# Kernel optimization log

Measured on AMD Instinct MI355X. Metric: run time of the kernel, lower is better.

## Reference

```python
import jax, jax.numpy as jnp
import numpy as np

# ---- config (matches init_kwargs) ----
B, S, V = 8, 900, 11
H, NH, HD = 512, 8, 64          # hidden, heads, head_dim = H // NH
L = 2                            # num_layers
EXPANSION = 4.0
INNER = 1536                     # find_multiple(round(4.0 * 512 * 2/3), 256)
STEPS = 2                        # mcmc_num_steps
EPS = 1e-5                       # rms_norm_eps
THETA = 10000.0                  # rope_theta
ESCALE = float(np.sqrt(H))       # embed_scale = sqrt(hidden_size)
SCALE = 1.0 / float(np.sqrt(HD))


def rms_norm(x):
    return x * jax.lax.rsqrt(jnp.mean(x * x, axis=-1, keepdims=True) + EPS)


def rope_tables():
    inv_freq = 1.0 / (THETA ** (jnp.arange(0, HD, 2, dtype=jnp.float32) / HD))
    t = jnp.arange(S, dtype=jnp.float32)
    freqs = jnp.outer(t, inv_freq)                # (S, HD/2)
    emb = jnp.concatenate([freqs, freqs], axis=-1)  # (S, HD)
    return jnp.cos(emb), jnp.sin(emb)


def rotate_half(x):
    x1, x2 = jnp.split(x, 2, axis=-1)
    return jnp.concatenate([-x2, x1], axis=-1)


def apply_rope(q, k, cos, sin):
    cos = cos[None, :, None, :]  # (1,S,1,HD) broadcast over batch & heads
    sin = sin[None, :, None, :]
    return q * cos + rotate_half(q) * sin, k * cos + rotate_half(k) * sin


def block(h, qkv_w, o_w, gu_w, d_w, cos, sin):
    b, s, _ = h.shape
    qkv = (h @ qkv_w).reshape(b, s, 3 * NH, HD)
    q, k, v = qkv[:, :, :NH], qkv[:, :, NH:2 * NH], qkv[:, :, 2 * NH:]
    q, k = apply_rope(q, k, cos, sin)
    scores = jnp.einsum('bqhd,bkhd->bhqk', q, k) * SCALE
    attn = jax.nn.softmax(scores, axis=-1)
    out = jnp.einsum('bhqk,bkhd->bqhd', attn, v).reshape(b, s, NH * HD)
    h = rms_norm(h + out @ o_w)                   # post-norm residual
    gu = h @ gu_w
    gate, up = gu[..., :INNER], gu[..., INNER:]
    h = rms_norm(h + (jax.nn.silu(gate) * up) @ d_w)
    return h


def energy(logits, embed_w, energy_w, qkv_w, o_w, gu_w, d_w, input_emb, cos, sin):
    probs = jax.nn.softmax(logits, axis=-1)       # soft token distribution
    h = input_emb + ESCALE * (probs @ embed_w)    # soft embedding
    for i in range(L):
        h = block(h, qkv_w[i], o_w[i], gu_w[i], d_w[i], cos, sin)
    return jnp.sum(h @ energy_w)                  # scalar energy


def setup_inputs() -> dict:
    key = jax.random.key(0)
    ks = jax.random.split(key, 8)
    inputs = jax.random.randint(ks[0], (B, S), 0, V, dtype=jnp.int64)
    puzzle_identifiers = jax.random.randint(ks[1], (B,), 0, 1, dtype=jnp.int64)
    init_std = 1.0 / ESCALE
    embed_w = jax.random.normal(ks[2], (V, H), jnp.float32) * init_std
    energy_w = jax.random.normal(ks[3], (H, 1), jnp.float32) * 0.02
    qkv_w = jax.random.normal(ks[4], (L, H, 3 * NH * HD), jnp.float32) * 0.02
    o_w = jax.random.normal(ks[5], (L, NH * HD, H), jnp.float32) * 0.02
    gu_w = jax.random.normal(ks[6], (L, H, 2 * INNER), jnp.float32) * 0.02
    d_w = jax.random.normal(ks[7], (L, INNER, H), jnp.float32) * 0.02
    alpha = jnp.asarray(100.0, jnp.float32)       # mcmc_step_size
    return {"inputs": inputs, "puzzle_identifiers": puzzle_identifiers,
            "embed_w": embed_w, "energy_w": energy_w, "qkv_w": qkv_w,
            "o_w": o_w, "gu_w": gu_w, "d_w": d_w, "alpha": alpha}


def reference(inputs, puzzle_identifiers, embed_w, energy_w, qkv_w, o_w, gu_w, d_w, alpha):
    cos, sin = rope_tables()
    input_emb = ESCALE * embed_w[inputs]          # (B,S,H)
    a = jnp.maximum(alpha, 1e-4)                  # torch.clamp(alpha, min=1e-4)
    logits = jnp.zeros((inputs.shape[0], S, V), jnp.float32)
    egrad = jax.grad(energy)
    for _ in range(STEPS):                        # MCMC energy-descent loop
        g = egrad(logits, embed_w, energy_w, qkv_w, o_w, gu_w, d_w, input_emb, cos, sin)
        logits = logits - a * g
    return logits
```

## Files before the change

### kernel.cpp

```cpp
#include <hip/hip_runtime.h>
#include <math.h>

#define B_ 8
#define S_ 900
#define V_ 11
#define H_ 512
#define NH_ 8
#define HD_ 64
#define INNER_ 1536
#define STEPS_ 2
#define NTOK (B_*S_)
#define EPS_ 1e-5f
#define THETA_ 10000.0f
#define ESCALE_ 22.627416997969522f
#define SCALE_ 0.125f
#define PT_ 68

typedef __attribute__((ext_vector_type(8))) short bh8;
typedef __attribute__((ext_vector_type(4))) float f32x4;
typedef __attribute__((ext_vector_type(4))) unsigned short us4;

union bfu { bh8 v; unsigned short s[8]; us4 q[2]; };

__device__ inline unsigned short f2bf(float x) {
  unsigned u = __builtin_bit_cast(unsigned, x);
  return (unsigned short)((u + 0x7FFFu + ((u >> 16) & 1u)) >> 16);
}
__device__ inline float b2f(unsigned short s) {
  return __builtin_bit_cast(float, (unsigned)s << 16);
}

__device__ inline void gld16(const unsigned short* g, unsigned short* l) {
  __builtin_amdgcn_global_load_lds(
      (const __attribute__((address_space(1))) void*)(g),
      (__attribute__((address_space(3))) void*)(l), 16, 0, 0);
}

__device__ inline bh8 lds16(const unsigned short* p) {
  bfu u;
  u.q[0] = *(const us4*)p;
  u.q[1] = *(const us4*)(p + 4);
  return u.v;
}
__device__ inline void sts16(unsigned short* p, bfu u) {
  *(us4*)p = u.q[0];
  *(us4*)(p + 4) = u.q[1];
}

__device__ inline float wave_sum64(float x) {
#pragma unroll
  for (int off = 32; off > 0; off >>= 1) x += __shfl_xor(x, off, 64);
  return x;
}


__global__ void k_zero(float* p, int n) {
  int i = blockIdx.x * blockDim.x + threadIdx.x;
  if (i < n) p[i] = 0.f;
}

__global__ void k_rope_tables(float* cs, float* sn) {
  int idx = blockIdx.x * blockDim.x + threadIdx.x;
  if (idx >= S_ * 32) return;
  int s = idx >> 5, i = idx & 31;
  float freq = powf(THETA_, -(float)i / 32.0f);
  float ang = (float)s * freq;
  cs[idx] = cosf(ang);
  sn[idx] = sinf(ang);
}

template <int DOSM>
__global__ void k_h0(const float* __restrict__ logits, float* __restrict__ P,
                     const float* __restrict__ E,
                     const int* __restrict__ inp, float* __restrict__ h0,
                     unsigned short* __restrict__ h016) {
  int t = blockIdx.x;
  int tid = threadIdx.x;
  __shared__ float p[V_];
  __shared__ int iw;
  if (DOSM) {
    if (tid == 0) {
      float x[V_];
      float m = -1e30f;
#pragma unroll
      for (int v = 0; v < V_; ++v) { x[v] = logits[t * V_ + v]; m = fmaxf(m, x[v]); }
      float ssum = 0.f;
#pragma unroll
      for (int v = 0; v < V_; ++v) { x[v] = __expf(x[v] - m); ssum += x[v]; }
      float inv = 1.f / ssum;
#pragma unroll
      for (int v = 0; v < V_; ++v) {
        float pv = x[v] * inv;
        p[v] = pv;
        P[t * V_ + v] = pv;
      }
    }
  } else {
    if (tid < V_) p[tid] = P[t * V_ + tid];
  }
  if (tid == 0) iw = inp[t];
  __syncthreads();
  for (int h = tid; h < H_; h += blockDim.x) {
    float acc = E[iw * H_ + h];
#pragma unroll
    for (int v = 0; v < V_; ++v) acc += p[v] * E[v * H_ + h];
    float val = ESCALE_ * acc;
    h0[(size_t)t * H_ + h] = val;
    h016[(size_t)t * H_ + h] = f2bf(val);
  }
}

__global__ void k_cast8(const float* __restrict__ X, unsigned short* __restrict__ Y, int n8) {
  int i = blockIdx.x * blockDim.x + threadIdx.x;
  if (i >= n8) return;
  const float4* p = (const float4*)(X + (size_t)i * 8);
  float4 a = p[0], b = p[1];
  bfu o;
  o.s[0] = f2bf(a.x); o.s[1] = f2bf(a.y); o.s[2] = f2bf(a.z); o.s[3] = f2bf(a.w);
  o.s[4] = f2bf(b.x); o.s[5] = f2bf(b.y); o.s[6] = f2bf(b.z); o.s[7] = f2bf(b.w);
  *(bh8*)(Y + (size_t)i * 8) = o.v;
}


__global__ void k_wt(const float* __restrict__ W, unsigned short* __restrict__ WT, int K, int N) {
  __shared__ float t[32][33];
  int k0 = blockIdx.y * 32, n0 = blockIdx.x * 32;
  int tx = threadIdx.x, ty = threadIdx.y;
#pragma unroll
  for (int i = 0; i < 4; ++i)
    t[ty + 8 * i][tx] = W[(size_t)(k0 + ty + 8 * i) * N + n0 + tx];
  __syncthreads();
#pragma unroll
  for (int i = 0; i < 4; ++i)
    WT[(size_t)(n0 + ty + 8 * i) * K + k0 + tx] = f2bf(t[tx][ty + 8 * i]);
}


template <int TM, int SILU_A, int ADD, int CBF, int ROPE, int SILUBWD>
__global__ __launch_bounds__(256) void k_gemm(const unsigned short* __restrict__ A16,
                                              const unsigned short* __restrict__ Bt,
                                              const float* __restrict__ Dm,
                                              float* __restrict__ Cf,
                                              unsigned short* __restrict__ C16,
                                              unsigned short* __restrict__ GU,
                                              const float* __restrict__ Cs,
                                              const float* __restrict__ Sn,
                                              int M, int N, int K, int lda) {
  __shared__ unsigned short As[2][TM][32];
  __shared__ unsigned short Bs[2][128][32];
  constexpr int FR = TM / 32;
  int tid = threadIdx.x;
  int m0 = blockIdx.y * TM, n0 = blockIdx.x * 128;
  int wid = tid >> 6, lane = tid & 63;
  int wr = (wid >> 1) * (FR * 16), wc = (wid & 1) * 64;
  int lr = lane & 15, lg = lane >> 4;
  int srow = lane >> 2, sck = (lane & 3) * 8;
  f32x4 acc[FR][4] = {};
  for (int k0 = 0; k0 < K; k0 += 64) {
    __syncthreads();
#pragma unroll
    for (int sub = 0; sub < 2; ++sub) {
      int kk = k0 + sub * 32;
#pragma unroll
      for (int half = 0; half < TM / 64; ++half) {
        if (SILU_A) {
          int row = (tid >> 2) + 64 * half;
          int ck = (tid & 3) * 8;
          int gr = m0 + row; gr = gr < M ? gr : M - 1;
          const unsigned short* src = &A16[(size_t)gr * lda + kk + ck];
          bfu pa;
#pragma unroll
          for (int j = 0; j < 8; ++j) {
            float g = b2f(src[j]), u = b2f(src[INNER_ + j]);
            pa.s[j] = f2bf((g / (1.f + __expf(-g))) * u);
          }
          *(bh8*)&As[sub][row][ck] = pa.v;
        } else {
          int gr = m0 + 64 * half + wid * 16 + srow; gr = gr < M ? gr : M - 1;
          gld16(&A16[(size_t)gr * lda + kk + sck], &As[sub][64 * half + wid * 16][0]);
        }
      }
#pragma unroll
      for (int i = 0; i < 2; ++i) {
        int bb = wid * 2 + i;
        gld16(&Bt[(size_t)(n0 + bb * 16 + srow) * K + kk + sck], &Bs[sub][bb * 16][0]);
      }
    }
    __syncthreads();
#pragma unroll
    for (int sub = 0; sub < 2; ++sub) {
      bh8 av[FR], bv[4];
#pragma unroll
      for (int fr = 0; fr < FR; ++fr) av[fr] = *(const bh8*)&As[sub][wr + fr * 16 + lr][lg * 8];
#pragma unroll
      for (int fc = 0; fc < 4; ++fc) bv[fc] = *(const bh8*)&Bs[sub][wc + fc * 16 + lr][lg * 8];
#pragma unroll
      for (int fr = 0; fr < FR; ++fr)
#pragma unroll
        for (int fc = 0; fc < 4; ++fc)
          acc[fr][fc] = __builtin_amdgcn_mfma_f32_16x16x32_bf16(av[fr], bv[fc], acc[fr][fc], 0, 0, 0);
    }
  }
  bool rope_on = ROPE && (((n0 + wc) >> 6) < 16);
#pragma unroll
  for (int fr = 0; fr < FR; ++fr) {
    int r0 = m0 + wr + fr * 16 + lg * 4;
#pragma unroll
    for (int i = 0; i < 4; ++i) {
      int gr = r0 + i;
      if (gr >= M) continue;
      float c0 = 1.f, s0 = 0.f, c1 = 1.f, s1 = 0.f;
      if (ROPE) {
        if (rope_on) {
          int s = gr % S_;
          c0 = Cs[s * 32 + lr];      s0 = Sn[s * 32 + lr];
          c1 = Cs[s * 32 + 16 + lr]; s1 = Sn[s * 32 + 16 + lr];
        }
      }
#pragma unroll
      for (int fc = 0; fc < 4; ++fc) {
        int gc = n0 + wc + fc * 16 + lr;
        float out = acc[fr][fc][i];
        if (ROPE) {
          float part = acc[fr][fc ^ 2][i];
          float cc = (fc & 1) ? c1 : c0;
          float ss = (fc & 1) ? s1 : s0;
          out = (fc < 2) ? (out * cc - part * ss) : (out * cc + part * ss);
        }
        if (ADD) out += Dm[(size_t)gr * N + gc];
        if (SILUBWD) {
          size_t gb = (size_t)gr * (size_t)(2 * INNER_) + gc;
          float g = b2f(GU[gb]), u = b2f(GU[gb + INNER_]);
          float sig = 1.f / (1.f + __expf(-g));
          GU[gb] = f2bf(out * u * sig * (1.f + g * (1.f - sig)));
          GU[gb + INNER_] = f2bf(out * g * sig);
        } else if (CBF) {
          C16[(size_t)gr * N + gc] = f2bf(out);
        } else {
          Cf[(size_t)gr * N + gc] = out;
        }
      }
    }
  }
}


__global__ __launch_bounds__(512) void k_attn_fwd3(const unsigned short* __restrict__ QKV,
                                                   unsigned short* __restrict__ AO,
                                                   float* __restrict__ MB,
                                                   float* __restrict__ LB) {
  __shared__ unsigned short Ks[64][PT_];
  __shared__ unsigned short VT[64][PT_];
  __shared__ unsigned short Ps[8][16][PT_];
  int tid = threadIdx.x;
  int h = blockIdx.y, b = blockIdx.z;
  int w = tid >> 6, lane = tid & 63;
  int lr = lane & 15, lg = lane >> 4;
  int q0 = blockIdx.x * 128 + w * 16;
  bool kRole = tid < 256;
  int t2 = kRole ? tid : tid - 256;
  int sr = t2 >> 2, sc0 = (t2 & 3) * 16;
  int vd0 = (t2 & 15) * 4, vk0 = (t2 >> 4) * 4;

  bh8 qf[2];
  {
    int qr = q0 + lr; if (qr >= S_) qr = S_ - 1;
    const unsigned short* qp = &QKV[((size_t)(b * S_ + qr) * 24 + h) * 64 + lg * 8];
    qf[0] = *(const bh8*)qp;
    qf[1] = *(const bh8*)(qp + 32);
  }
  f32x4 accO[4] = {};
  float m[4], lsum[4];
#pragma unroll
  for (int i = 0; i < 4; ++i) { m[i] = -1e30f; lsum[i] = 0.f; }

  bfu kA, kB;
  us4 vR[4];
  if (kRole) {
    int src = sr;
    size_t ts = (size_t)b * S_ + (src < S_ ? src : S_ - 1);
    const unsigned short* gp = &QKV[(ts * 24 + 8 + h) * 64 + sc0];
    kA.v = *(const bh8*)gp;
    kB.v = *(const bh8*)(gp + 8);
  } else {
#pragma unroll
    for (int j = 0; j < 4; ++j) {
      int s2 = vk0 + j;
      size_t t3 = (size_t)b * S_ + (s2 < S_ ? s2 : S_ - 1);
      vR[j] = *(const us4*)&QKV[(t3 * 24 + 16 + h) * 64 + vd0];
    }
  }

  for (int kt = 0; kt < S_; kt += 64) {
    __syncthreads();
    if (kRole) {
      sts16(&Ks[sr][sc0], kA);
      sts16(&Ks[sr][sc0 + 8], kB);
    } else {
#pragma unroll
      for (int dd = 0; dd < 4; ++dd) {
        us4 pk = {vR[0][dd], vR[1][dd], vR[2][dd], vR[3][dd]};
        *(us4*)&VT[vd0 + dd][vk0] = pk;
      }
    }
    __syncthreads();
    if (kt + 64 < S_) {
      if (kRole) {
        int src = kt + 64 + sr;
        size_t ts = (size_t)b * S_ + (src < S_ ? src : S_ - 1);
        const unsigned short* gp = &QKV[(ts * 24 + 8 + h) * 64 + sc0];
        kA.v = *(const bh8*)gp;
        kB.v = *(const bh8*)(gp + 8);
      } else {
#pragma unroll
        for (int j = 0; j < 4; ++j) {
          int s2 = kt + 64 + vk0 + j;
          size_t t3 = (size_t)b * S_ + (s2 < S_ ? s2 : S_ - 1);
          vR[j] = *(const us4*)&QKV[(t3 * 24 + 16 + h) * 64 + vd0];
        }
      }
    }
    f32x4 accS[4] = {};
#pragma unroll
    for (int ks = 0; ks < 2; ++ks)
#pragma unroll
      for (int fk = 0; fk < 4; ++fk)
        accS[fk] = __builtin_amdgcn_mfma_f32_16x16x32_bf16(qf[ks], lds16(&Ks[fk * 16 + lr][ks * 32 + lg * 8]), accS[fk], 0, 0, 0);
    float sc[4][4], pmax[4];
#pragma unroll
    for (int i = 0; i < 4; ++i) pmax[i] = -1e30f;
#pragma unroll
    for (int fk = 0; fk < 4; ++fk)
#pragma unroll
      for (int i = 0; i < 4; ++i) {
        float s = accS[fk][i] * SCALE_;
        if (kt + fk * 16 + lr >= S_) s = -1e30f;
        sc[fk][i] = s;
        pmax[i] = fmaxf(pmax[i], s);
      }
#pragma unroll
    for (int i = 0; i < 4; ++i) {
      float v = pmax[i];
      v = fmaxf(v, __shfl_xor(v, 1, 64));
      v = fmaxf(v, __shfl_xor(v, 2, 64));
      v = fmaxf(v, __shfl_xor(v, 4, 64));
      v = fmaxf(v, __shfl_xor(v, 8, 64));
      pmax[i] = v;
    }
    float psum[4];
#pragma unroll
    for (int i = 0; i < 4; ++i) {
      float mn = fmaxf(m[i], pmax[i]);
      float eo = __expf(m[i] - mn);
      m[i] = mn;
      lsum[i] *= eo;
#pragma unroll
      for (int fd = 0; fd < 4; ++fd) accO[fd][i] *= eo;
      psum[i] = 0.f;
    }
#pragma unroll
    for (int fk = 0; fk < 4; ++fk)
#pragma unroll
      for (int i = 0; i < 4; ++i) {
        float p = __expf(sc[fk][i] - m[i]);
        sc[fk][i] = p;
        psum[i] += p;
      }
#pragma unroll
    for (int i = 0; i < 4; ++i) {
      float v = psum[i];
      v += __shfl_xor(v, 1, 64);
      v += __shfl_xor(v, 2, 64);
      v += __shfl_xor(v, 4, 64);
      v += __shfl_xor(v, 8, 64);
      lsum[i] += v;
    }
#pragma unroll
    for (int fk = 0; fk < 4; ++fk)
#pragma unroll
      for (int i = 0; i < 4; ++i)
        Ps[w][lg * 4 + i][fk * 16 + lr] = f2bf(sc[fk][i]);
#pragma unroll
    for (int ks = 0; ks < 2; ++ks) {
      bh8 ap = lds16(&Ps[w][lr][ks * 32 + lg * 8]);
#pragma unroll
      for (int fd = 0; fd < 4; ++fd)
        accO[fd] = __builtin_amdgcn_mfma_f32_16x16x32_bf16(ap, lds16(&VT[fd * 16 + lr][ks * 32 + lg * 8]), accO[fd], 0, 0, 0);
    }
  }
#pragma unroll
  for (int i = 0; i < 4; ++i) {
    int q = q0 + lg * 4 + i;
    if (q < S_) {
      float linv = 1.f / lsum[i];
      size_t obase = (size_t)(b * S_ + q) * H_ + h * 64;
#pragma unroll
      for (int fd = 0; fd < 4; ++fd) AO[obase + fd * 16 + lr] = f2bf(accO[fd][i] * linv);
      if (lr == 0) {
        MB[((size_t)b * NH_ + h) * S_ + q] = m[i];
        LB[((size_t)b * NH_ + h) * S_ + q] = linv;
      }
    }
  }
}

__global__ __launch_bounds__(512) void k_attn_bwd_dq3(const unsigned short* __restrict__ QKV,
                                                      const unsigned short* __restrict__ O16,
                                                      const unsigned short* __restrict__ dO,
                                                      const float* __restrict__ MB,
                                                      const float* __restrict__ LB,
                                                      float* __restrict__ DB,
                                                      const float* __restrict__ Cs,
                                                      const float* __restrict__ Sn,
                                                      unsigned short* __restrict__ dQKV) {
  __shared__ unsigned short Ks[64][PT_];
  __shared__ unsigned short Vs[64][PT_];
  __shared__ unsigned short KT[64][PT_];
  __shared__ unsigned short Ps[8][16][PT_];
  int tid = threadIdx.x;
  int h = blockIdx.y, b = blockIdx.z;
  int w = tid >> 6, lane = tid & 63;
  int lr = lane & 15, lg = lane >> 4;
  int q0 = blockIdx.x * 128 + w * 16;
  size_t sbase = ((size_t)b * NH_ + h) * S_;
  bool kRole = tid < 256;
  int t2 = kRole ? tid : tid - 256;
  int sr = t2 >> 2, sc0 = (t2 & 3) * 16;
  int vd0 = (t2 & 15) * 4, vk0 = (t2 >> 4) * 4;

  bh8 qf[2], dof[2];
  float pd = 0.f;
  {
    int qr = q0 + lr; if (qr >= S_) qr = S_ - 1;
    const unsigned short* qp = &QKV[((size_t)(b * S_ + qr) * 24 + h) * 64 + lg * 8];
    const unsigned short* dp = &dO[(size_t)(b * S_ + qr) * H_ + h * 64 + lg * 8];
    const unsigned short* op = &O16[(size_t)(b * S_ + qr) * H_ + h * 64 + lg * 8];
    qf[0] = *(const bh8*)qp;  qf[1] = *(const bh8*)(qp + 32);
    dof[0] = *(const bh8*)dp; dof[1] = *(const bh8*)(dp + 32);
    bfu o0, o1, d0, d1;
    o0.v = *(const bh8*)op; o1.v = *(const bh8*)(op + 32);
    d0.v = dof[0]; d1.v = dof[1];
#pragma unroll
    for (int j = 0; j < 8; ++j)
      pd += b2f(o0.s[j]) * b2f(d0.s[j]) + b2f(o1.s[j]) * b2f(d1.s[j]);
    pd += __shfl_xor(pd, 16, 64);
    pd += __shfl_xor(pd, 32, 64);
    if (lg == 0 && q0 + lr < S_) DB[sbase + q0 + lr] = pd;
  }
  float mrow[4], lrow[4], drow[4];
#pragma unroll
  for (int i = 0; i < 4; ++i) {
    int q = q0 + lg * 4 + i; if (q >= S_) q = S_ - 1;
    mrow[i] = MB[sbase + q];
    lrow[i] = LB[sbase + q];
    drow[i] = __shfl(pd, lg * 4 + i, 64);
  }
  f32x4 accQ[4] = {};

  bfu pA{}, pB{}, pC{}, pD{};
  us4 rv[4];
  if (kRole) {
    int src = sr;
    bool vld = src < S_;
    size_t ts = (size_t)b * S_ + (vld ? src : S_ - 1);
    const unsigned short* kp = &QKV[(ts * 24 + 8 + h) * 64 + sc0];
    if (vld) {
      pA.v = *(const bh8*)kp;
      pB.v = *(const bh8*)(kp + 8);
      pC.v = *(const bh8*)(kp + 512);
      pD.v = *(const bh8*)(kp + 520);
    }
  } else {
#pragma unroll
    for (int j = 0; j < 4; ++j) {
      int s2 = vk0 + j;
      bool v2 = s2 < S_;
      size_t t3 = (size_t)b * S_ + (v2 ? s2 : S_ - 1);
      us4 t = *(const us4*)&QKV[(t3 * 24 + 8 + h) * 64 + vd0];
      if (!v2) t = us4{0, 0, 0, 0};
      rv[j] = t;
    }
  }

  for (int kt = 0; kt < S_; kt += 64) {
    __syncthreads();
    if (kRole) {
      sts16(&Ks[sr][sc0], pA); sts16(&Ks[sr][sc0 + 8], pB);
      sts16(&Vs[sr][sc0], pC); sts16(&Vs[sr][sc0 + 8], pD);
    } else {
#pragma unroll
      for (int dd = 0; dd < 4; ++dd) {
        us4 pk = {rv[0][dd], rv[1][dd], rv[2][dd], rv[3][dd]};
        *(us4*)&KT[vd0 + dd][vk0] = pk;
      }
    }
    __syncthreads();
    if (kt + 64 < S_) {
      if (kRole) {
        int src = kt + 64 + sr;
        bool vld = src < S_;
        size_t ts = (size_t)b * S_ + (vld ? src : S_ - 1);
        const unsigned short* kp = &QKV[(ts * 24 + 8 + h) * 64 + sc0];
        pA = bfu{}; pB = bfu{}; pC = bfu{}; pD = bfu{};
        if (vld) {
          pA.v = *(const bh8*)kp;
          pB.v = *(const bh8*)(kp + 8);
          pC.v = *(const bh8*)(kp + 512);
          pD.v = *(const bh8*)(kp + 520);
        }
      } else {
#pragma unroll
        for (int j = 0; j < 4; ++j) {
          int s2 = kt + 64 + vk0 + j;
          bool v2 = s2 < S_;
          size_t t3 = (size_t)b * S_ + (v2 ? s2 : S_ - 1);
          us4 t = *(const us4*)&QKV[(t3 * 24 + 8 + h) * 64 + vd0];
          if (!v2) t = us4{0, 0, 0, 0};
          rv[j] = t;
        }
      }
    }
    f32x4 aS[4] = {}, aD[4] = {};
#pragma unroll
    for (int ks = 0; ks < 2; ++ks)
#pragma unroll
      for (int fk = 0; fk < 4; ++fk) {
        aS[fk] = __builtin_amdgcn_mfma_f32_16x16x32_bf16(qf[ks], lds16(&Ks[fk * 16 + lr][ks * 32 + lg * 8]), aS[fk], 0, 0, 0);
        aD[fk] = __builtin_amdgcn_mfma_f32_16x16x32_bf16(dof[ks], lds16(&Vs[fk * 16 + lr][ks * 32 + lg * 8]), aD[fk], 0, 0, 0);
      }
#pragma unroll
    for (int fk = 0; fk < 4; ++fk)
#pragma unroll
      for (int i = 0; i < 4; ++i) {
        float p = __expf(aS[fk][i] * SCALE_ - mrow[i]) * lrow[i];
        float ds = p * (aD[fk][i] - drow[i]);
        Ps[w][lg * 4 + i][fk * 16 + lr] = f2bf(ds);
      }
#pragma unroll
    for (int ks = 0; ks < 2; ++ks) {
      bh8 ap = lds16(&Ps[w][lr][ks * 32 + lg * 8]);
#pragma unroll
      for (int fd = 0; fd < 4; ++fd)
        accQ[fd] = __builtin_amdgcn_mfma_f32_16x16x32_bf16(ap, lds16(&KT[fd * 16 + lr][ks * 32 + lg * 8]), accQ[fd], 0, 0, 0);
    }
  }
#pragma unroll
  for (int i = 0; i < 4; ++i) {
    int q = q0 + lg * 4 + i;
    if (q < S_) {
      size_t obase = ((size_t)(b * S_ + q) * 24 + h) * 64;
      float c0 = Cs[q * 32 + lr], s0 = Sn[q * 32 + lr];
      float c1 = Cs[q * 32 + 16 + lr], s1 = Sn[q * 32 + 16 + lr];
#pragma unroll
      for (int fd = 0; fd < 4; ++fd) {
        float x = SCALE_ * accQ[fd][i];
        float p = SCALE_ * accQ[fd ^ 2][i];
        float cc = (fd & 1) ? c1 : c0;
        float ss = (fd & 1) ? s1 : s0;
        float out = (fd < 2) ? (x * cc + p * ss) : (x * cc - p * ss);
        dQKV[obase + fd * 16 + lr] = f2bf(out);
      }
    }
  }
}

__global__ __launch_bounds__(512) void k_attn_bwd_kv3(const unsigned short* __restrict__ QKV,
                                                      const unsigned short* __restrict__ dO,
                                                      const float* __restrict__ MB,
                                                      const float* __restrict__ LB,
                                                      const float* __restrict__ DB,
                                                      const float* __restrict__ Cs,
                                                      const float* __restrict__ Sn,
                                                      unsigned short* __restrict__ dQKV) {
  __shared__ unsigned short Qs[64][PT_];
  __shared__ unsigned short dOs[64][PT_];
  __shared__ unsigned short QT[64][PT_];
  __shared__ unsigned short dOT[64][PT_];
  __shared__ unsigned short Ps[8][16][PT_];
  __shared__ float sM[64], sL[64], sD[64];
  int tid = threadIdx.x;
  int h = blockIdx.y, b = blockIdx.z;
  int w = tid >> 6, lane = tid & 63;
  int lr = lane & 15, lg = lane >> 4;
  int k0w = blockIdx.x * 128 + w * 16;
  size_t sbase = ((size_t)b * NH_ + h) * S_;
  bool kRole = tid < 256;
  int t2 = kRole ? tid : tid - 256;
  int sr = t2 >> 2, sc0 = (t2 & 3) * 16;
  int vd0 = (t2 & 15) * 4, vk0 = (t2 >> 4) * 4;

  bh8 kf[2], vf[2];
  {
    int kr = k0w + lr; if (kr >= S_) kr = S_ - 1;
    const unsigned short* kp = &QKV[((size_t)(b * S_ + kr) * 24 + 8 + h) * 64 + lg * 8];
    kf[0] = *(const bh8*)kp;        kf[1] = *(const bh8*)(kp + 32);
    vf[0] = *(const bh8*)(kp + 512); vf[1] = *(const bh8*)(kp + 544);
  }
  f32x4 accK[4] = {}, accV[4] = {};

  bfu pA{}, pB{}, pC{}, pD{};
  us4 rq[4], rd[4];
  float stM = 0.f, stL = 0.f, stD = 0.f;
  if (kRole) {
    int src = sr;
    bool vld = src < S_;
    size_t ts = (size_t)b * S_ + (vld ? src : S_ - 1);
    const unsigned short* qp = &QKV[(ts * 24 + h) * 64 + sc0];
    const unsigned short* dp = &dO[ts * H_ + h * 64 + sc0];
    pA.v = *(const bh8*)qp;
    pB.v = *(const bh8*)(qp + 8);
    if (vld) {
      pC.v = *(const bh8*)dp;
      pD.v = *(const bh8*)(dp + 8);
    }
    if (tid < 64) {
      bool v2 = tid < S_;
      int sc = v2 ? tid : S_ - 1;
      stM = MB[sbase + sc];
      stL = LB[sbase + sc];
      stD = v2 ? DB[sbase + sc] : 0.f;
    }
  } else {
#pragma unroll
    for (int j = 0; j < 4; ++j) {
      int s2 = vk0 + j;
      bool v2 = s2 < S_;
      size_t t3 = (size_t)b * S_ + (v2 ? s2 : S_ - 1);
      rq[j] = *(const us4*)&QKV[(t3 * 24 + h) * 64 + vd0];
      us4 td = *(const us4*)&dO[t3 * H_ + h * 64 + vd0];
      if (!v2) td = us4{0, 0, 0, 0};
      rd[j] = td;
    }
  }

  for (int qt = 0; qt < S_; qt += 64) {
    __syncthreads();
    if (kRole) {
      sts16(&Qs[sr][sc0], pA);  sts16(&Qs[sr][sc0 + 8], pB);
      sts16(&dOs[sr][sc0], pC); sts16(&dOs[sr][sc0 + 8], pD);
      if (tid < 64) {
        sM[tid] = stM;
        sL[tid] = stL;
        sD[tid] = stD;
      }
    } else {
#pragma unroll
      for (int dd = 0; dd < 4; ++dd) {
        us4 pq = {rq[0][dd], rq[1][dd], rq[2][dd], rq[3][dd]};
        us4 pd = {rd[0][dd], rd[1][dd], rd[2][dd], rd[3][dd]};
        *(us4*)&QT[vd0 + dd][vk0] = pq;
        *(us4*)&dOT[vd0 + dd][vk0] = pd;
      }
    }
    __syncthreads();
    if (qt + 64 < S_) {
      if (kRole) {
        int src = qt + 64 + sr;
        bool vld = src < S_;
        size_t ts = (size_t)b * S_ + (vld ? src : S_ - 1);
        const unsigned short* qp = &QKV[(ts * 24 + h) * 64 + sc0];
        const unsigned short* dp = &dO[ts * H_ + h * 64 + sc0];
        pA.v = *(const bh8*)qp;
        pB.v = *(const bh8*)(qp + 8);
        pC = bfu{}; pD = bfu{};
        if (vld) {
          pC.v = *(const bh8*)dp;
          pD.v = *(const bh8*)(dp + 8);
        }
        if (tid < 64) {
          int s2 = qt + 64 + tid;
          bool v2 = s2 < S_;
          int sc = v2 ? s2 : S_ - 1;
          stM = MB[sbase + sc];
          stL = LB[sbase + sc];
          stD = v2 ? DB[sbase + sc] : 0.f;
        }
      } else {
#pragma unroll
        for (int j = 0; j < 4; ++j) {
          int s2 = qt + 64 + vk0 + j;
          bool v2 = s2 < S_;
          size_t t3 = (size_t)b * S_ + (v2 ? s2 : S_ - 1);
          rq[j] = *(const us4*)&QKV[(t3 * 24 + h) * 64 + vd0];
          us4 td = *(const us4*)&dO[t3 * H_ + h * 64 + vd0];
          if (!v2) td = us4{0, 0, 0, 0};
          rd[j] = td;
        }
      }
    }
    f32x4 aS[4] = {}, aD[4] = {};
#pragma unroll
    for (int ks = 0; ks < 2; ++ks)
#pragma unroll
      for (int fq = 0; fq < 4; ++fq) {
        aS[fq] = __builtin_amdgcn_mfma_f32_16x16x32_bf16(kf[ks], lds16(&Qs[fq * 16 + lr][ks * 32 + lg * 8]), aS[fq], 0, 0, 0);
        aD[fq] = __builtin_amdgcn_mfma_f32_16x16x32_bf16(vf[ks], lds16(&dOs[fq * 16 + lr][ks * 32 + lg * 8]), aD[fq], 0, 0, 0);
      }
    float pv[4][4];
#pragma unroll
    for (int fq = 0; fq < 4; ++fq) {
      float mq = sM[fq * 16 + lr], lq = sL[fq * 16 + lr];
#pragma unroll
      for (int i = 0; i < 4; ++i) {
        float p = __expf(aS[fq][i] * SCALE_ - mq) * lq;
        pv[fq][i] = p;
        Ps[w][lg * 4 + i][fq * 16 + lr] = f2bf(p);
      }
    }
#pragma unroll
    for (int qs = 0; qs < 2; ++qs) {
      bh8 ap = lds16(&Ps[w][lr][qs * 32 + lg * 8]);
#pragma unroll
      for (int fd = 0; fd < 4; ++fd)
        accV[fd] = __builtin_amdgcn_mfma_f32_16x16x32_bf16(ap, lds16(&dOT[fd * 16 + lr][qs * 32 + lg * 8]), accV[fd], 0, 0, 0);
    }
#pragma unroll
    for (int fq = 0; fq < 4; ++fq) {
      float dq = sD[fq * 16 + lr];
#pragma unroll
      for (int i = 0; i < 4; ++i)
        Ps[w][lg * 4 + i][fq * 16 + lr] = f2bf(pv[fq][i] * (aD[fq][i] - dq));
    }
#pragma unroll
    for (int qs = 0; qs < 2; ++qs) {
      bh8 ap = lds16(&Ps[w][lr][qs * 32 + lg * 8]);
#pragma unroll
      for (int fd = 0; fd < 4; ++fd)
        accK[fd] = __builtin_amdgcn_mfma_f32_16x16x32_bf16(ap, lds16(&QT[fd * 16 + lr][qs * 32 + lg * 8]), accK[fd], 0, 0, 0);
    }
  }
#pragma unroll
  for (int i = 0; i < 4; ++i) {
    int k = k0w + lg * 4 + i;
    if (k < S_) {
      size_t obase = ((size_t)(b * S_ + k) * 24 + 8 + h) * 64;
      float c0 = Cs[k * 32 + lr], s0 = Sn[k * 32 + lr];
      float c1 = Cs[k * 32 + 16 + lr], s1 = Sn[k * 32 + 16 + lr];
#pragma unroll
      for (int fd = 0; fd < 4; ++fd) {
        float x = SCALE_ * accK[fd][i];
        float p = SCALE_ * accK[fd ^ 2][i];
        float cc = (fd & 1) ? c1 : c0;
        float ss = (fd & 1) ? s1 : s0;
        float out = (fd < 2) ? (x * cc + p * ss) : (x * cc - p * ss);
        dQKV[obase + fd * 16 + lr] = f2bf(out);
        dQKV[obase + 512 + fd * 16 + lr] = f2bf(accV[fd][i]);
      }
    }
  }
}


__global__ __launch_bounds__(256) void k_rms_fwd(const float* __restrict__ X, float* __restrict__ Y,
                                                 unsigned short* __restrict__ Y16) {
  int t = blockIdx.x, tid = threadIdx.x;
  float x0 = X[(size_t)t * H_ + tid], x1 = X[(size_t)t * H_ + tid + 256];
  __shared__ float red[256];
  red[tid] = x0 * x0 + x1 * x1;
  __syncthreads();
  for (int s = 128; s > 0; s >>= 1) {
    if (tid < s) red[tid] += red[tid + s];
    __syncthreads();
  }
  float r = rsqrtf(red[0] / H_ + EPS_);
  float y0 = x0 * r, y1 = x1 * r;
  Y[(size_t)t * H_ + tid] = y0;
  Y[(size_t)t * H_ + tid + 256] = y1;
  Y16[(size_t)t * H_ + tid] = f2bf(y0);
  Y16[(size_t)t * H_ + tid + 256] = f2bf(y1);
}

template <int EWB>
__global__ __launch_bounds__(256) void k_rms_bwd(const float* __restrict__ X,
                                                 const float* __restrict__ GY,
                                                 const float* __restrict__ EW,
                                                 float* __restrict__ GX,
                                                 unsigned short* __restrict__ GX16) {
  int t = blockIdx.x, tid = threadIdx.x;
  float x0 = X[(size_t)t * H_ + tid], x1 = X[(size_t)t * H_ + tid + 256];
  float g0, g1;
  if (EWB) {
    g0 = EW[tid];
    g1 = EW[tid + 256];
  } else {
    g0 = GY[(size_t)t * H_ + tid];
    g1 = GY[(size_t)t * H_ + tid + 256];
  }
  __shared__ float r1[256], r2[256];
  r1[tid] = x0 * x0 + x1 * x1;
  r2[tid] = x0 * g0 + x1 * g1;
  __syncthreads();
  for (int s = 128; s > 0; s >>= 1) {
    if (tid < s) { r1[tid] += r1[tid + s]; r2[tid] += r2[tid + s]; }
    __syncthreads();
  }
  float r = rsqrtf(r1[0] / H_ + EPS_);
  float coef = r * r * r * r2[0] / (float)H_;
  float o0 = r * g0 - coef * x0, o1 = r * g1 - coef * x1;
  GX[(size_t)t * H_ + tid] = o0;
  GX[(size_t)t * H_ + tid + 256] = o1;
  GX16[(size_t)t * H_ + tid] = f2bf(o0);
  GX16[(size_t)t * H_ + tid + 256] = f2bf(o1);
}


__global__ __launch_bounds__(64) void k_logits_update(const float* __restrict__ G,
                                                      const float* __restrict__ E,
                                                      const float* __restrict__ P,
                                                      const float* __restrict__ alpha,
                                                      float* __restrict__ logits) {
  int t = blockIdx.x, lane = threadIdx.x;
  float dp[V_];
#pragma unroll
  for (int v = 0; v < V_; ++v) dp[v] = 0.f;
  for (int hh = lane; hh < H_; hh += 64) {
    float gh = G[(size_t)t * H_ + hh];
#pragma unroll
    for (int v = 0; v < V_; ++v) dp[v] += gh * E[v * H_ + hh];
  }
#pragma unroll
  for (int v = 0; v < V_; ++v) dp[v] = wave_sum64(dp[v]) * ESCALE_;
  float dot = 0.f;
  float pv[V_];
#pragma unroll
  for (int v = 0; v < V_; ++v) {
    pv[v] = P[t * V_ + v];
    dot += pv[v] * dp[v];
  }
  float a = fmaxf(alpha[0], 1e-4f);
  if (lane < V_) logits[t * V_ + lane] -= a * pv[lane] * (dp[lane] - dot);
}


struct Ctx {
  unsigned short *Q16, *Q016, *dQ16, *GU16, *DO16, *AO16, *AO016, *X116, *UDX16, *U016;
  float *X1, *X2, *X20, *G, *UDX, *P, *MB, *LB, *DB, *MB0, *LB0, *CS, *SN;
  const float* EW;
  const unsigned short *WTqkv[2], *WTo[2], *WTgu[2], *WTd[2];
  const unsigned short *WSqkv[2], *WSo[2], *WSgu[2], *WSd[2];
  hipStream_t st;
};

static void block_forward(Ctx& c, int l, const float* hin, const unsigned short* hin16,
                          float* hout, unsigned short* qb, unsigned short* ao,
                          float* mb, float* lb, float* x2buf, unsigned short* u16buf) {
  k_gemm<128, 0, 0, 1, 1, 0><<<dim3(3 * H_ / 128, (NTOK + 127) / 128), 256, 0, c.st>>>(
      hin16, c.WTqkv[l], nullptr, nullptr, qb, nullptr, c.CS, c.SN, NTOK, 3 * H_, H_, H_);
  k_attn_fwd3<<<dim3((S_ + 127) / 128, NH_, B_), 512, 0, c.st>>>(qb, ao, mb, lb);
  k_gemm<64, 0, 1, 0, 0, 0><<<dim3(H_ / 128, (NTOK + 63) / 64), 256, 0, c.st>>>(
      ao, c.WTo[l], hin, c.X1, nullptr, nullptr, nullptr, nullptr, NTOK, H_, H_, H_);
  k_rms_fwd<<<NTOK, 256, 0, c.st>>>(c.X1, c.UDX, u16buf);
  k_gemm<128, 0, 0, 1, 0, 0><<<dim3(2 * INNER_ / 128, (NTOK + 127) / 128), 256, 0, c.st>>>(
      u16buf, c.WTgu[l], nullptr, nullptr, c.GU16, nullptr, nullptr, nullptr, NTOK, 2 * INNER_, H_, H_);
  k_gemm<64, 1, 1, 0, 0, 0><<<dim3(H_ / 128, (NTOK + 63) / 64), 256, 0, c.st>>>(
      c.GU16, c.WTd[l], c.UDX, x2buf, nullptr, nullptr, nullptr, nullptr, NTOK, H_, INNER_, 2 * INNER_);
  if (hout) k_rms_fwd<<<NTOK, 256, 0, c.st>>>(x2buf, hout, c.UDX16);
}

static void block_backward(Ctx& c, int l, const float* hin, const unsigned short* hin16,
                           unsigned short* qb, unsigned short* ao, float* mb, float* lb,
                           bool full) {
  const float* x2src;
  if (full) {
    block_forward(c, l, hin, hin16, nullptr, qb, ao, mb, lb, c.X2, c.UDX16);
    x2src = c.X2;
  } else {
    k_gemm<64, 0, 1, 0, 0, 0><<<dim3(H_ / 128, (NTOK + 63) / 64), 256, 0, c.st>>>(
        ao, c.WTo[l], hin, c.X1, nullptr, nullptr, nullptr, nullptr, NTOK, H_, H_, H_);
    k_gemm<128, 0, 0, 1, 0, 0><<<dim3(2 * INNER_ / 128, (NTOK + 127) / 128), 256, 0, c.st>>>(
        c.U016, c.WTgu[l], nullptr, nullptr, c.GU16, nullptr, nullptr, nullptr, NTOK, 2 * INNER_, H_, H_);
    x2src = c.X20;
  }
  if (full)
    k_rms_bwd<1><<<NTOK, 256, 0, c.st>>>(x2src, nullptr, c.EW, c.UDX, c.UDX16);
  else
    k_rms_bwd<0><<<NTOK, 256, 0, c.st>>>(x2src, c.G, nullptr, c.UDX, c.UDX16);
  k_gemm<128, 0, 0, 0, 0, 1><<<dim3(INNER_ / 128, (NTOK + 127) / 128), 256, 0, c.st>>>(
      c.UDX16, c.WSd[l], nullptr, nullptr, nullptr, c.GU16, nullptr, nullptr, NTOK, INNER_, H_, H_);
  k_gemm<64, 0, 1, 0, 0, 0><<<dim3(H_ / 128, (NTOK + 63) / 64), 256, 0, c.st>>>(
      c.GU16, c.WSgu[l], c.UDX, c.G, nullptr, nullptr, nullptr, nullptr, NTOK, H_, 2 * INNER_, 2 * INNER_);
  k_rms_bwd<0><<<NTOK, 256, 0, c.st>>>(c.X1, c.G, nullptr, c.UDX, c.UDX16);
  k_gemm<64, 0, 0, 1, 0, 0><<<dim3(H_ / 128, (NTOK + 63) / 64), 256, 0, c.st>>>(
      c.UDX16, c.WSo[l], nullptr, nullptr, c.DO16, nullptr, nullptr, nullptr, NTOK, H_, H_, H_);
  dim3 agrid128((S_ + 127) / 128, NH_, B_);
  k_attn_bwd_dq3<<<agrid128, 512, 0, c.st>>>(qb, ao, c.DO16, mb, lb, c.DB, c.CS, c.SN, c.dQ16);
  k_attn_bwd_kv3<<<agrid128, 512, 0, c.st>>>(qb, c.DO16, mb, lb, c.DB, c.CS, c.SN, c.dQ16);
  k_gemm<64, 0, 1, 0, 0, 0><<<dim3(H_ / 128, (NTOK + 63) / 64), 256, 0, c.st>>>(
      c.dQ16, c.WSqkv[l], c.UDX, c.G, nullptr, nullptr, nullptr, nullptr, NTOK, H_, 3 * H_, 3 * H_);
}

extern "C" void kernel_launch(void* const* d_in, const int* in_sizes, int n_in,
                              void* d_out, int out_size, void* d_ws, size_t ws_size,
                              hipStream_t stream) {
  const int* inputs = (const int*)d_in[0];
  const float* E = (const float*)d_in[2];
  const float* ew = (const float*)d_in[3];
  const float* qkvw = (const float*)d_in[4];
  const float* ow = (const float*)d_in[5];
  const float* guw = (const float*)d_in[6];
  const float* dw = (const float*)d_in[7];
  const float* alpha = (const float*)d_in[8];
  float* logits = (float*)d_out;

  const size_t WT_FLOATS = 3407872;
  const size_t NEED =
      3 * ((size_t)NTOK * 3 * H_ / 2) +
      ((size_t)NTOK * INNER_) +
      5 * ((size_t)NTOK * H_) +
      6 * ((size_t)NTOK * H_ / 2) +
      ((size_t)NTOK * V_) +
      5 * ((size_t)B_ * NH_ * S_) +
      2 * ((size_t)S_ * 32) +
      2 * WT_FLOATS;
  if (ws_size < NEED * sizeof(float)) {
    k_zero<<<(NTOK * V_ + 255) / 256, 256, 0, stream>>>(logits, NTOK * V_);
    return;
  }

  float* f = (float*)d_ws;
  Ctx c;
  c.st = stream;
  c.EW = ew;
  c.Q16 = (unsigned short*)f;  f += (size_t)NTOK * 3 * H_ / 2;
  c.Q016 = (unsigned short*)f; f += (size_t)NTOK * 3 * H_ / 2;
  c.dQ16 = (unsigned short*)f; f += (size_t)NTOK * 3 * H_ / 2;
  c.GU16 = (unsigned short*)f; f += (size_t)NTOK * INNER_;
  c.X1 = f;   f += (size_t)NTOK * H_;
  c.X2 = f;   f += (size_t)NTOK * H_;
  c.X20 = f;  f += (size_t)NTOK * H_;
  c.G = f;    f += (size_t)NTOK * H_;
  c.UDX = f;  f += (size_t)NTOK * H_;
  c.AO16 = (unsigned short*)f;  f += (size_t)NTOK * H_ / 2;
  c.AO016 = (unsigned short*)f; f += (size_t)NTOK * H_ / 2;
  c.DO16 = (unsigned short*)f;  f += (size_t)NTOK * H_ / 2;
  c.X116 = (unsigned short*)f;  f += (size_t)NTOK * H_ / 2;
  c.UDX16 = (unsigned short*)f; f += (size_t)NTOK * H_ / 2;
  c.U016 = (unsigned short*)f;  f += (size_t)NTOK * H_ / 2;
  c.P = f;    f += (size_t)NTOK * V_;
  c.MB = f;   f += (size_t)B_ * NH_ * S_;
  c.LB = f;   f += (size_t)B_ * NH_ * S_;
  c.DB = f;   f += (size_t)B_ * NH_ * S_;
  c.MB0 = f;  f += (size_t)B_ * NH_ * S_;
  c.LB0 = f;  f += (size_t)B_ * NH_ * S_;
  c.CS = f;   f += (size_t)S_ * 32;
  c.SN = f;   f += (size_t)S_ * 32;
  unsigned short* wt = (unsigned short*)f;

  const size_t LQKV = (size_t)H_ * 3 * H_;
  const size_t LO = (size_t)H_ * H_;
  const size_t LGU = (size_t)H_ * 2 * INNER_;
  const size_t LD = (size_t)INNER_ * H_;

  for (int l = 0; l < 2; ++l) {
    c.WTqkv[l] = wt;
    k_wt<<<dim3(3 * H_ / 32, H_ / 32), dim3(32, 8), 0, stream>>>(qkvw + l * LQKV, wt, H_, 3 * H_);
    wt += LQKV;
    c.WTo[l] = wt;
    k_wt<<<dim3(H_ / 32, H_ / 32), dim3(32, 8), 0, stream>>>(ow + l * LO, wt, H_, H_);
    wt += LO;
    c.WTgu[l] = wt;
    k_wt<<<dim3(2 * INNER_ / 32, H_ / 32), dim3(32, 8), 0, stream>>>(guw + l * LGU, wt, H_, 2 * INNER_);
    wt += LGU;
    c.WTd[l] = wt;
    k_wt<<<dim3(H_ / 32, INNER_ / 32), dim3(32, 8), 0, stream>>>(dw + l * LD, wt, INNER_, H_);
    wt += LD;
  }
  {
    unsigned short* ws = wt;
    k_cast8<<<(int)((2 * LQKV / 8 + 255) / 256), 256, 0, stream>>>(qkvw, ws, (int)(2 * LQKV / 8));
    c.WSqkv[0] = ws; c.WSqkv[1] = ws + LQKV; ws += 2 * LQKV;
    k_cast8<<<(int)((2 * LO / 8 + 255) / 256), 256, 0, stream>>>(ow, ws, (int)(2 * LO / 8));
    c.WSo[0] = ws; c.WSo[1] = ws + LO; ws += 2 * LO;
    k_cast8<<<(int)((2 * LGU / 8 + 255) / 256), 256, 0, stream>>>(guw, ws, (int)(2 * LGU / 8));
    c.WSgu[0] = ws; c.WSgu[1] = ws + LGU; ws += 2 * LGU;
    k_cast8<<<(int)((2 * LD / 8 + 255) / 256), 256, 0, stream>>>(dw, ws, (int)(2 * LD / 8));
    c.WSd[0] = ws; c.WSd[1] = ws + LD;
  }

  k_zero<<<(NTOK * V_ + 255) / 256, 256, 0, stream>>>(logits, NTOK * V_);
  k_rope_tables<<<(S_ * 32 + 255) / 256, 256, 0, stream>>>(c.CS, c.SN);

  for (int step = 0; step < STEPS_; ++step) {
    k_h0<1><<<NTOK, 256, 0, stream>>>(logits, c.P, E, inputs, c.X1, c.X116);
    block_forward(c, 0, c.X1, c.X116, c.UDX, c.Q016, c.AO016, c.MB0, c.LB0, c.X20, c.U016);
    block_backward(c, 1, c.UDX, c.UDX16, c.Q16, c.AO16, c.MB, c.LB, true);
    k_h0<0><<<NTOK, 256, 0, stream>>>(nullptr, c.P, E, inputs, c.X1, c.X116);
    block_backward(c, 0, c.X1, c.X116, c.Q016, c.AO016, c.MB0, c.LB0, false);
    k_logits_update<<<NTOK, 64, 0, stream>>>(c.G, E, c.P, alpha, logits);
  }
}
```

Measured before the change: 2.264 ms.

## Double-buffer GEMM K loop and split P/dS LDS tiles in attention backward

The GEMM main loop now prefetches the next 32-wide K slice into the other LDS buffer while MFMAs run on the current one, with one barrier per step in place of two per 64-wide step. The goal is to overlap global-to-LDS traffic with compute. In the attention KV backward kernel, P and dS are written to separate LDS tiles so the dV and dK MFMAs can be interleaved in one loop without rewriting Ps in between. The cost is an extra 16x68 bf16 tile per warp in LDS, and the GEMM now has half as much work between barriers.

```diff
diff --git a/kernel.cpp b/kernel.cpp
--- a/kernel.cpp
+++ b/kernel.cpp
@@ -156,50 +156,51 @@
   int lr = lane & 15, lg = lane >> 4;
   int srow = lane >> 2, sck = (lane & 3) * 8;
   f32x4 acc[FR][4] = {};
-  for (int k0 = 0; k0 < K; k0 += 64) {
+
+  auto stage = [&](int buf, int kk) {
+#pragma unroll
+    for (int half = 0; half < TM / 64; ++half) {
+      if (SILU_A) {
+        int row = (tid >> 2) + 64 * half;
+        int ck = (tid & 3) * 8;
+        int gr = m0 + row; gr = gr < M ? gr : M - 1;
+        const unsigned short* src = &A16[(size_t)gr * lda + kk + ck];
+        bfu pa;
+#pragma unroll
+        for (int j = 0; j < 8; ++j) {
+          float g = b2f(src[j]), u = b2f(src[INNER_ + j]);
+          pa.s[j] = f2bf((g / (1.f + __expf(-g))) * u);
+        }
+        *(bh8*)&As[buf][row][ck] = pa.v;
+      } else {
+        int gr = m0 + 64 * half + wid * 16 + srow; gr = gr < M ? gr : M - 1;
+        gld16(&A16[(size_t)gr * lda + kk + sck], &As[buf][64 * half + wid * 16][0]);
+      }
+    }
+#pragma unroll
+    for (int i = 0; i < 2; ++i) {
+      int bb = wid * 2 + i;
+      gld16(&Bt[(size_t)(n0 + bb * 16 + srow) * K + kk + sck], &Bs[buf][bb * 16][0]);
+    }
+  };
+
+  stage(0, 0);
+  __syncthreads();
+  int nk = K >> 5;
+  for (int t = 0; t < nk; ++t) {
+    int cur = t & 1;
+    if (t + 1 < nk) stage(cur ^ 1, (t + 1) << 5);
+    bh8 av[FR], bv[4];
+#pragma unroll
+    for (int fr = 0; fr < FR; ++fr) av[fr] = *(const bh8*)&As[cur][wr + fr * 16 + lr][lg * 8];
+#pragma unroll
+    for (int fc = 0; fc < 4; ++fc) bv[fc] = *(const bh8*)&Bs[cur][wc + fc * 16 + lr][lg * 8];
+#pragma unroll
+    for (int fr = 0; fr < FR; ++fr)
+#pragma unroll
+      for (int fc = 0; fc < 4; ++fc)
+        acc[fr][fc] = __builtin_amdgcn_mfma_f32_16x16x32_bf16(av[fr], bv[fc], acc[fr][fc], 0, 0, 0);
     __syncthreads();
-#pragma unroll
-    for (int sub = 0; sub < 2; ++sub) {
-      int kk = k0 + sub * 32;
-#pragma unroll
-      for (int half = 0; half < TM / 64; ++half) {
-        if (SILU_A) {
-          int row = (tid >> 2) + 64 * half;
-          int ck = (tid & 3) * 8;
-          int gr = m0 + row; gr = gr < M ? gr : M - 1;
-          const unsigned short* src = &A16[(size_t)gr * lda + kk + ck];
-          bfu pa;
-#pragma unroll
-          for (int j = 0; j < 8; ++j) {
-            float g = b2f(src[j]), u = b2f(src[INNER_ + j]);
-            pa.s[j] = f2bf((g / (1.f + __expf(-g))) * u);
-          }
-          *(bh8*)&As[sub][row][ck] = pa.v;
-        } else {
-          int gr = m0 + 64 * half + wid * 16 + srow; gr = gr < M ? gr : M - 1;
-          gld16(&A16[(size_t)gr * lda + kk + sck], &As[sub][64 * half + wid * 16][0]);
-        }
-      }
-#pragma unroll
-      for (int i = 0; i < 2; ++i) {
-        int bb = wid * 2 + i;
-        gld16(&Bt[(size_t)(n0 + bb * 16 + srow) * K + kk + sck], &Bs[sub][bb * 16][0]);
-      }
-    }
-    __syncthreads();
-#pragma unroll
-    for (int sub = 0; sub < 2; ++sub) {
-      bh8 av[FR], bv[4];
-#pragma unroll
-      for (int fr = 0; fr < FR; ++fr) av[fr] = *(const bh8*)&As[sub][wr + fr * 16 + lr][lg * 8];
-#pragma unroll
-      for (int fc = 0; fc < 4; ++fc) bv[fc] = *(const bh8*)&Bs[sub][wc + fc * 16 + lr][lg * 8];
-#pragma unroll
-      for (int fr = 0; fr < FR; ++fr)
-#pragma unroll
-        for (int fc = 0; fc < 4; ++fc)
-          acc[fr][fc] = __builtin_amdgcn_mfma_f32_16x16x32_bf16(av[fr], bv[fc], acc[fr][fc], 0, 0, 0);
-    }
   }
   bool rope_on = ROPE && (((n0 + wc) >> 6) < 16);
 #pragma unroll
@@ -577,6 +578,7 @@
   __shared__ unsigned short QT[64][PT_];
   __shared__ unsigned short dOT[64][PT_];
   __shared__ unsigned short Ps[8][16][PT_];
+  __shared__ unsigned short Ds[8][16][PT_];
   __shared__ float sM[64], sL[64], sD[64];
   int tid = threadIdx.x;
   int h = blockIdx.y, b = blockIdx.z;
@@ -696,37 +698,25 @@
         aS[fq] = __builtin_amdgcn_mfma_f32_16x16x32_bf16(kf[ks], lds16(&Qs[fq * 16 + lr][ks * 32 + lg * 8]), aS[fq], 0, 0, 0);
         aD[fq] = __builtin_amdgcn_mfma_f32_16x16x32_bf16(vf[ks], lds16(&dOs[fq * 16 + lr][ks * 32 + lg * 8]), aD[fq], 0, 0, 0);
       }
-    float pv[4][4];
 #pragma unroll
     for (int fq = 0; fq < 4; ++fq) {
-      float mq = sM[fq * 16 + lr], lq = sL[fq * 16 + lr];
+      float mq = sM[fq * 16 + lr], lq = sL[fq * 16 + lr], dq = sD[fq * 16 + lr];
 #pragma unroll
       for (int i = 0; i < 4; ++i) {
         float p = __expf(aS[fq][i] * SCALE_ - mq) * lq;
-        pv[fq][i] = p;
         Ps[w][lg * 4 + i][fq * 16 + lr] = f2bf(p);
+        Ds[w][lg * 4 + i][fq * 16 + lr] = f2bf(p * (aD[fq][i] - dq));
       }
     }
 #pragma unroll
     for (int qs = 0; qs < 2; ++qs) {
       bh8 ap = lds16(&Ps[w][lr][qs * 32 + lg * 8]);
-#pragma unroll
-      for (int fd = 0; fd < 4; ++fd)
+      bh8 ad = lds16(&Ds[w][lr][qs * 32 + lg * 8]);
+#pragma unroll
+      for (int fd = 0; fd < 4; ++fd) {
         accV[fd] = __builtin_amdgcn_mfma_f32_16x16x32_bf16(ap, lds16(&dOT[fd * 16 + lr][qs * 32 + lg * 8]), accV[fd], 0, 0, 0);
-    }
-#pragma unroll
-    for (int fq = 0; fq < 4; ++fq) {
-      float dq = sD[fq * 16 + lr];
-#pragma unroll
-      for (int i = 0; i < 4; ++i)
-        Ps[w][lg * 4 + i][fq * 16 + lr] = f2bf(pv[fq][i] * (aD[fq][i] - dq));
-    }
-#pragma unroll
-    for (int qs = 0; qs < 2; ++qs) {
-      bh8 ap = lds16(&Ps[w][lr][qs * 32 + lg * 8]);
-#pragma unroll
-      for (int fd = 0; fd < 4; ++fd)
-        accK[fd] = __builtin_amdgcn_mfma_f32_16x16x32_bf16(ap, lds16(&QT[fd * 16 + lr][qs * 32 + lg * 8]), accK[fd], 0, 0, 0);
+        accK[fd] = __builtin_amdgcn_mfma_f32_16x16x32_bf16(ad, lds16(&QT[fd * 16 + lr][qs * 32 + lg * 8]), accK[fd], 0, 0, 0);
+      }
     }
   }
 #pragma unroll
```

Result: no change. 2.247 ms (-0.7%).
